# Performance work log

Measured on AMD Instinct MI355X. Metric: run time of the kernel, lower is better.

The kernel has to match this reference:

```python
import jax, jax.numpy as jnp
import numpy as np

N_HEAD = 16
ROPE_BASE = 10000.0


def _rope(x, cos, sin):
    # x: [B,H,T,D]; cos/sin: [T,D/2] broadcast over B,H
    half = x.shape[-1] // 2
    x1, x2 = x[..., :half], x[..., half:]
    return jnp.concatenate([x1 * cos - x2 * sin, x1 * sin + x2 * cos], axis=-1)


def setup_inputs() -> dict:
    key = jax.random.key(0)
    k1, k2, k3 = jax.random.split(key, 3)
    C = 2048
    x = jax.random.normal(k1, (4, 2048, C), dtype=jnp.float32)
    w_qkv = jax.random.normal(k2, (C, 3 * C), dtype=jnp.float32) * 0.02
    w_proj = jax.random.normal(k3, (C, C), dtype=jnp.float32) * 0.02
    return {"x": x, "w_qkv": w_qkv, "w_proj": w_proj}


def reference(x, w_qkv, w_proj):
    B, T, C = x.shape
    H = N_HEAD
    D = C // H
    half = D // 2

    qkv = x @ w_qkv  # [B,T,3C]
    q, k, v = jnp.split(qkv, 3, axis=-1)
    # [B,T,C] -> [B,H,T,D]
    q = q.reshape(B, T, H, D).transpose(0, 2, 1, 3)
    k = k.reshape(B, T, H, D).transpose(0, 2, 1, 3)
    v = v.reshape(B, T, H, D).transpose(0, 2, 1, 3)

    # RoPE cache (start_pos = 0, no kv_cache / prefill path)
    inv_freq = 1.0 / (ROPE_BASE ** (jnp.arange(half, dtype=jnp.float32) / half))
    pos = jnp.arange(T, dtype=jnp.float32)
    freqs = pos[:, None] * inv_freq[None, :]  # [T, half]
    cos, sin = jnp.cos(freqs), jnp.sin(freqs)

    q = _rope(q, cos, sin)
    k = _rope(k, cos, sin)

    # scaled dot-product attention with explicit causal mask
    att = jnp.einsum("bhqd,bhkd->bhqk", q, k) / jnp.sqrt(jnp.asarray(D, x.dtype))
    causal = jnp.arange(T)[:, None] >= jnp.arange(T)[None, :]  # [T,T] bool
    att = jnp.where(causal, att, jnp.asarray(-jnp.inf, att.dtype))
    att = jax.nn.softmax(att, axis=-1)
    # dropout = identity (eval mode)
    out = jnp.einsum("bhqk,bhkd->bhqd", att, v)
    out = out.transpose(0, 2, 1, 3).reshape(B, T, C)
    out = out @ w_proj
    return out, k, v  # (output, new kv-cache)
```

## Files before the change

### kernel.cpp

```cpp
#include <hip/hip_runtime.h>
#include <math.h>

#define CDIM 2048
#define TDIM 2048
#define BDIM 4
#define HDIM 16
#define DDIM 128
#define M1   (BDIM * TDIM)
#define N1   (3 * CDIM)
#define KK   CDIM
#define NT   32

typedef unsigned short u16;
typedef __bf16 bf16x8 __attribute__((ext_vector_type(8)));
typedef float f32x4 __attribute__((ext_vector_type(4)));

__device__ __forceinline__ u16 f2b(float f) {
  union { float f; unsigned u; } x; x.f = f;
  unsigned r = x.u + 0x7fffu + ((x.u >> 16) & 1u);
  return (u16)(r >> 16);
}

__device__ __forceinline__ void gload_lds16(const void* g, void* l) {
  __builtin_amdgcn_global_load_lds(
      (__attribute__((address_space(1))) void*)g,
      (__attribute__((address_space(3))) void*)l, 16, 0, 0);
}

__global__ void convert_x(const float* __restrict__ x, u16* __restrict__ xb, int n4) {
  int i = blockIdx.x * blockDim.x + threadIdx.x;
  if (i < n4) {
    float4 v = ((const float4*)x)[i];
    unsigned long long o = (unsigned long long)f2b(v.x)
                         | ((unsigned long long)f2b(v.y) << 16)
                         | ((unsigned long long)f2b(v.z) << 32)
                         | ((unsigned long long)f2b(v.w) << 48);
    ((unsigned long long*)xb)[i] = o;
  }
}

__global__ void transpose_w(const float* __restrict__ w, u16* __restrict__ wt, int K, int N) {
  __shared__ float tile[32][33];
  const int n0 = blockIdx.x * 32, k0 = blockIdx.y * 32;
  const int tx = threadIdx.x & 31, ty = threadIdx.x >> 5;
  for (int r = ty; r < 32; r += 8)
    tile[r][tx] = w[(k0 + r) * N + n0 + tx];
  __syncthreads();
  for (int r = ty; r < 32; r += 8)
    wt[(n0 + r) * K + k0 + tx] = f2b(tile[tx][r]);
}

__global__ void rope_tab(float* __restrict__ cosT, float* __restrict__ sinT) {
  int i = blockIdx.x * blockDim.x + threadIdx.x;
  int t = i >> 6, d = i & 63;
  double inv = pow(10000.0, -(double)d / 64.0);
  double a = (double)t * inv;
  cosT[i] = (float)cos(a);
  sinT[i] = (float)sin(a);
}

__global__ void transpose_v(const float* __restrict__ v, u16* __restrict__ vt) {
  __shared__ float tile[32][33];
  const int bh = blockIdx.z;
  const int t0 = blockIdx.x * 32, d0 = blockIdx.y * 32;
  const int tx = threadIdx.x & 31, ty = threadIdx.x >> 5;
  const float* src = v + (bh * TDIM + t0) * DDIM + d0;
  for (int r = ty; r < 32; r += 8)
    tile[r][tx] = src[r * DDIM + tx];
  __syncthreads();
  u16* dst = vt + (bh * DDIM + d0) * TDIM + t0;
  for (int r = ty; r < 32; r += 8)
    dst[r * TDIM + tx] = f2b(tile[tx][r]);
}


#define GEMM256_MAINLOOP(APTR, BPTR)                                           \
  const int rA = lane >> 3, cA = lane & 7;                                     \
  const int stgrow = wave * 8 + rA;                                            \
  const int stgoff = stgrow * KK + ((cA ^ rA) * 8);                            \
  const u16* Ag = (APTR) + m0 * KK + stgoff;                                   \
  const u16* Bg = (BPTR) + n0 * KK + stgoff;                                   \
  const int ldsw = wave * 512;                                  \
  f32x4 acc[8][4];                                                             \
  {                                                                            \
    f32x4 z = {0.f, 0.f, 0.f, 0.f};                                            \
    _Pragma("unroll")                                                          \
    for (int i = 0; i < 8; ++i)                                                \
      _Pragma("unroll")                                                        \
      for (int j = 0; j < 4; ++j) acc[i][j] = z;                               \
  }                                                                            \
                                         \
  _Pragma("unroll")                                                            \
  for (int i = 0; i < 4; ++i) {                                                \
    gload_lds16(Ag + i * 64 * KK, &lds[i * 4096 + ldsw]);                      \
    gload_lds16(Bg + i * 64 * KK, &lds[32768 + i * 4096 + ldsw]);              \
  }                                                                            \
  __syncthreads();                                                             \
  const int rsw = c16 & 7;                               \
  for (int kt = 0; kt < NT; ++kt) {                                            \
    const int cur = kt & 1;                                                    \
    const u16* bufA = &lds[cur * 16384];                                       \
    const u16* bufB = &lds[32768 + cur * 16384];                               \
    u16* nA = &lds[(cur ^ 1) * 16384];                                         \
    u16* nB = &lds[32768 + (cur ^ 1) * 16384];                                 \
    const u16* Agn = Ag + (kt + 1) * 64;                                       \
    const u16* Bgn = Bg + (kt + 1) * 64;                                       \
    const bool pre = (kt + 1 < NT);                                            \
    bf16x8 afr[4][2], bfr[2][2], bfr2[2][2];                                   \
                                          \
    _Pragma("unroll")                                                          \
    for (int i = 0; i < 4; ++i)                                                \
      _Pragma("unroll")                                                        \
      for (int kh = 0; kh < 2; ++kh)                                           \
        afr[i][kh] = *(const bf16x8*)&bufA[(wm + i * 16 + c16) * 64 +          \
                                           (((kh * 4 + quad) ^ rsw) * 8)];     \
    _Pragma("unroll")                                                          \
    for (int j = 0; j < 2; ++j)                                                \
      _Pragma("unroll")                                                        \
      for (int kh = 0; kh < 2; ++kh)                                           \
        bfr[j][kh] = *(const bf16x8*)&bufB[(wn + j * 16 + c16) * 64 +          \
                                           (((kh * 4 + quad) ^ rsw) * 8)];     \
    if (pre) {                                                                 \
      _Pragma("unroll")                                                        \
      for (int i = 0; i < 4; ++i)                                              \
        gload_lds16(Agn + i * 64 * KK, &nA[i * 4096 + ldsw]);                  \
    }                                                                          \
    __builtin_amdgcn_s_barrier();                                              \
    asm volatile("s_waitcnt lgkmcnt(0)" ::: "memory");                         \
    __builtin_amdgcn_s_setprio(1);                                             \
    _Pragma("unroll")                                                          \
    for (int i = 0; i < 4; ++i)                                                \
      _Pragma("unroll")                                                        \
      for (int j = 0; j < 2; ++j)                                              \
        _Pragma("unroll")                                                      \
        for (int kh = 0; kh < 2; ++kh)                                         \
          acc[i][j] = __builtin_amdgcn_mfma_f32_16x16x32_bf16(                 \
              afr[i][kh], bfr[j][kh], acc[i][j], 0, 0, 0);                     \
    __builtin_amdgcn_s_setprio(0);                                             \
    __builtin_amdgcn_s_barrier();                                              \
                                          \
    _Pragma("unroll")                                                          \
    for (int j = 0; j < 2; ++j)                                                \
      _Pragma("unroll")                                                        \
      for (int kh = 0; kh < 2; ++kh)                                           \
        bfr2[j][kh] = *(const bf16x8*)&bufB[(wn + (2 + j) * 16 + c16) * 64 +   \
                                            (((kh * 4 + quad) ^ rsw) * 8)];    \
    if (pre) {                                                                 \
      _Pragma("unroll")                                                        \
      for (int i = 0; i < 4; ++i)                                              \
        gload_lds16(Bgn + i * 64 * KK, &nB[i * 4096 + ldsw]);                  \
    }                                                                          \
    __builtin_amdgcn_s_barrier();                                              \
    asm volatile("s_waitcnt lgkmcnt(0)" ::: "memory");                         \
    __builtin_amdgcn_s_setprio(1);                                             \
    _Pragma("unroll")                                                          \
    for (int i = 0; i < 4; ++i)                                                \
      _Pragma("unroll")                                                        \
      for (int j = 0; j < 2; ++j)                                              \
        _Pragma("unroll")                                                      \
        for (int kh = 0; kh < 2; ++kh)                                         \
          acc[i][2 + j] = __builtin_amdgcn_mfma_f32_16x16x32_bf16(             \
              afr[i][kh], bfr2[j][kh], acc[i][2 + j], 0, 0, 0);                \
    __builtin_amdgcn_s_setprio(0);                                             \
    __builtin_amdgcn_s_barrier();                                              \
                                          \
    _Pragma("unroll")                                                          \
    for (int i = 0; i < 4; ++i)                                                \
      _Pragma("unroll")                                                        \
      for (int kh = 0; kh < 2; ++kh)                                           \
        afr[i][kh] = *(const bf16x8*)&bufA[(wm + (4 + i) * 16 + c16) * 64 +    \
                                           (((kh * 4 + quad) ^ rsw) * 8)];     \
    __builtin_amdgcn_s_barrier();                                              \
    asm volatile("s_waitcnt lgkmcnt(0)" ::: "memory");                         \
    __builtin_amdgcn_s_setprio(1);                                             \
    _Pragma("unroll")                                                          \
    for (int i = 0; i < 4; ++i)                                                \
      _Pragma("unroll")                                                        \
      for (int j = 0; j < 2; ++j)                                              \
        _Pragma("unroll")                                                      \
        for (int kh = 0; kh < 2; ++kh)                                         \
          acc[4 + i][2 + j] = __builtin_amdgcn_mfma_f32_16x16x32_bf16(         \
              afr[i][kh], bfr2[j][kh], acc[4 + i][2 + j], 0, 0, 0);            \
    __builtin_amdgcn_s_setprio(0);                                             \
    __builtin_amdgcn_s_barrier();                                              \
                                          \
    _Pragma("unroll")                                                          \
    for (int j = 0; j < 2; ++j)                                                \
      _Pragma("unroll")                                                        \
      for (int kh = 0; kh < 2; ++kh)                                           \
        bfr[j][kh] = *(const bf16x8*)&bufB[(wn + j * 16 + c16) * 64 +          \
                                           (((kh * 4 + quad) ^ rsw) * 8)];     \
    __builtin_amdgcn_s_barrier();                                              \
    asm volatile("s_waitcnt lgkmcnt(0)" ::: "memory");                         \
    __builtin_amdgcn_s_setprio(1);                                             \
    _Pragma("unroll")                                                          \
    for (int i = 0; i < 4; ++i)                                                \
      _Pragma("unroll")                                                        \
      for (int j = 0; j < 2; ++j)                                              \
        _Pragma("unroll")                                                      \
        for (int kh = 0; kh < 2; ++kh)                                         \
          acc[4 + i][j] = __builtin_amdgcn_mfma_f32_16x16x32_bf16(             \
              afr[i][kh], bfr[j][kh], acc[4 + i][j], 0, 0, 0);                 \
    __builtin_amdgcn_s_setprio(0);                                             \
        \
    __syncthreads();                                                           \
  }

__global__ __launch_bounds__(512, 2) void gemm_qkv(
    const u16* __restrict__ A,
    const u16* __restrict__ Bt,
    const float* __restrict__ cosT, const float* __restrict__ sinT,
    u16* __restrict__ qb, u16* __restrict__ kb,
    float* __restrict__ kout, float* __restrict__ vout)
{
  extern __shared__ __align__(16) u16 lds[];
  const int tid = threadIdx.x, wave = tid >> 6, lane = tid & 63;
  const int quad = lane >> 4, c16 = lane & 15;
  const int bid = blockIdx.y * 24 + blockIdx.x;
  const int swz = (bid & 7) * 96 + (bid >> 3);
  const int m0 = (swz / 24) * 256, n0 = (swz % 24) * 256;
  const int wm = (wave >> 2) * 128, wn = (wave & 3) * 64;

  GEMM256_MAINLOOP(A, Bt)

  float* cbuf = (float*)lds;
  const int mat = n0 >> 11;
  const int hbase = (n0 & 2047) >> 7;
  const float qscale = 0.088388347648318447f;
#pragma unroll
  for (int pass = 0; pass < 4; ++pass) {
    __syncthreads();
    if ((wave >> 2) == (pass >> 1)) {
#pragma unroll
      for (int i = 0; i < 4; ++i) {
        const int mf = (pass & 1) * 4 + i;
#pragma unroll
        for (int j = 0; j < 4; ++j)
#pragma unroll
          for (int r = 0; r < 4; ++r)
            cbuf[(i * 16 + quad * 4 + r) * 260 + wn + j * 16 + c16] = acc[mf][j][r];
      }
    }
    __syncthreads();
#pragma unroll
    for (int it = 0; it < 16; ++it) {
      int p = it * 512 + tid;
      int lr = p >> 7;
      int hc = (p >> 6) & 1;
      int d = p & 63;
      float x1 = cbuf[lr * 260 + hc * 128 + d];
      float x2 = cbuf[lr * 260 + hc * 128 + 64 + d];
      int mg = m0 + pass * 64 + lr;
      int b = mg >> 11, t = mg & 2047;
      int h = hbase + hc;
      int idx = ((b * HDIM + h) * TDIM + t) * DDIM + d;
      if (mat == 2) {
        vout[idx] = x1; vout[idx + 64] = x2;
      } else {
        float cs = cosT[t * 64 + d], sn = sinT[t * 64 + d];
        float o1 = x1 * cs - x2 * sn;
        float o2 = x1 * sn + x2 * cs;
        if (mat == 0) {
          qb[idx] = f2b(o1 * qscale); qb[idx + 64] = f2b(o2 * qscale);
        } else {
          kout[idx] = o1; kout[idx + 64] = o2;
          kb[idx] = f2b(o1); kb[idx + 64] = f2b(o2);
        }
      }
    }
  }
}

__global__ __launch_bounds__(512, 2) void gemm_proj(
    const u16* __restrict__ A,
    const u16* __restrict__ Bt,
    float* __restrict__ out)
{
  extern __shared__ __align__(16) u16 lds[];
  const int tid = threadIdx.x, wave = tid >> 6, lane = tid & 63;
  const int quad = lane >> 4, c16 = lane & 15;
  const int bid = blockIdx.y * 8 + blockIdx.x;
  const int swz = (bid & 7) * 32 + (bid >> 3);
  const int m0 = (swz >> 3) * 256, n0 = (swz & 7) * 256;
  const int wm = (wave >> 2) * 128, wn = (wave & 3) * 64;

  GEMM256_MAINLOOP(A, Bt)

#pragma unroll
  for (int mf = 0; mf < 8; ++mf)
#pragma unroll
    for (int nf = 0; nf < 4; ++nf)
#pragma unroll
      for (int r = 0; r < 4; ++r)
        out[(m0 + wm + mf * 16 + quad * 4 + r) * CDIM + n0 + wn + nf * 16 + c16] =
            acc[mf][nf][r];
}

__global__ __launch_bounds__(256, 2) void attn(
    const u16* __restrict__ qb, const u16* __restrict__ kb,
    const u16* __restrict__ vt, u16* __restrict__ att)
{
  __shared__ __attribute__((aligned(16))) u16 sh[24576];
  u16* const ksm = sh;
  u16* const vsm = sh + 8192;
  u16* const psm = sh + 16384;

  const int tid = threadIdx.x, wave = tid >> 6, lane = tid & 63;
  const int quad = lane >> 4, c16 = lane & 15;
  const int bx = blockIdx.x;
  const int bh = blockIdx.y;

  for (int hv = 0; hv < 2; ++hv) {
    const int qt = hv ? (7 - bx) : (bx + 8);
    const int q0 = qt * 128;

    {
      const u16* qg = qb + (bh * TDIM + q0) * DDIM;
      const int rowl = wave * 4 + (lane >> 4);
      const int ch = lane & 15;
#pragma unroll
      for (int r = 0; r < 8; ++r) {
        int row = r * 16 + rowl;
        gload_lds16(qg + row * DDIM + (ch ^ (row & 15)) * 8,
                    &sh[(r * 16 + wave * 4) * 128]);
      }
    }
    __syncthreads();
    bf16x8 qf[2][4];
#pragma unroll
    for (int g = 0; g < 2; ++g)
#pragma unroll
      for (int kp = 0; kp < 4; ++kp)
        qf[g][kp] = *(const bf16x8*)&sh[(g * 64 + wave * 16 + c16) * 128 +
                                        (((kp * 4 + quad) ^ c16) * 8)];
    __syncthreads();

    f32x4 o[2][8];
    f32x4 zero = {0.f, 0.f, 0.f, 0.f};
#pragma unroll
    for (int g = 0; g < 2; ++g)
#pragma unroll
      for (int jd = 0; jd < 8; ++jd) o[g][jd] = zero;
    float mrow[2][4], lrow[2][4];
#pragma unroll
    for (int g = 0; g < 2; ++g)
#pragma unroll
      for (int r = 0; r < 4; ++r) { mrow[g][r] = -INFINITY; lrow[g][r] = 0.f; }

    const int nchunk = 2 * qt + 2;
    for (int kc = 0; kc < nchunk; ++kc) {
      const int kc0 = kc * 64;
      {
        const u16* kg = kb + (bh * TDIM + kc0) * DDIM;
        const int rowl = wave * 4 + (lane >> 4);
        const int ch = lane & 15;
#pragma unroll
        for (int r = 0; r < 4; ++r) {
          int row = r * 16 + rowl;
          gload_lds16(kg + row * DDIM + (ch ^ (row & 15)) * 8,
                      &ksm[(r * 16 + wave * 4) * 128]);
        }
        const u16* vg = vt + bh * (DDIM * TDIM) + kc0;
        const int rowv = wave * 8 + (lane >> 3);
        const int chv = lane & 7;
#pragma unroll
        for (int r = 0; r < 4; ++r) {
          int row = r * 32 + rowv;
          gload_lds16(vg + row * TDIM + (chv ^ (row & 7)) * 8,
                      &vsm[(r * 32 + wave * 8) * 64]);
        }
      }
      __syncthreads();

      f32x4 st[2][4];
#pragma unroll
      for (int g = 0; g < 2; ++g)
#pragma unroll
        for (int j = 0; j < 4; ++j) st[g][j] = zero;
#pragma unroll
      for (int kp = 0; kp < 4; ++kp) {
#pragma unroll
        for (int j = 0; j < 4; ++j) {
          bf16x8 bk = *(const bf16x8*)&ksm[(j * 16 + c16) * 128 +
                                           (((kp * 4 + quad) ^ c16) * 8)];
          st[0][j] = __builtin_amdgcn_mfma_f32_16x16x32_bf16(qf[0][kp], bk, st[0][j], 0, 0, 0);
          st[1][j] = __builtin_amdgcn_mfma_f32_16x16x32_bf16(qf[1][kp], bk, st[1][j], 0, 0, 0);
        }
      }

      u16* const pw = psm + wave * 2048;
      float al2[2][4];
#pragma unroll
      for (int g = 0; g < 2; ++g) {
        const bool dg = (kc >= 2 * qt + g);
        const int qrow_base = q0 + g * 64 + wave * 16 + quad * 4;
#pragma unroll
        for (int r = 0; r < 4; ++r) {
          float mx = -INFINITY;
#pragma unroll
          for (int j = 0; j < 4; ++j) {
            float sv = st[g][j][r];
            if (dg && (kc0 + j * 16 + c16 > qrow_base + r)) sv = -INFINITY;
            st[g][j][r] = sv;
            mx = fmaxf(mx, sv);
          }
          mx = fmaxf(mx, __shfl_xor(mx, 1, 64));
          mx = fmaxf(mx, __shfl_xor(mx, 2, 64));
          mx = fmaxf(mx, __shfl_xor(mx, 4, 64));
          mx = fmaxf(mx, __shfl_xor(mx, 8, 64));
          float mnew = fmaxf(mrow[g][r], mx);
          float al = __expf(mrow[g][r] - mnew);
          mrow[g][r] = mnew;
          al2[g][r] = al;
          float sum = 0.f;
          const int row16 = quad * 4 + r;
#pragma unroll
          for (int j = 0; j < 4; ++j) {
            float p = __expf(st[g][j][r] - mnew);
            sum += p;
            int chunk = (j * 2 + (c16 >> 3)) ^ (row16 & 7);
            pw[g * 1024 + row16 * 64 + chunk * 8 + (c16 & 7)] = f2b(p);
          }
          sum += __shfl_xor(sum, 1, 64);
          sum += __shfl_xor(sum, 2, 64);
          sum += __shfl_xor(sum, 4, 64);
          sum += __shfl_xor(sum, 8, 64);
          lrow[g][r] = lrow[g][r] * al + sum;
        }
#pragma unroll
        for (int jd = 0; jd < 8; ++jd)
#pragma unroll
          for (int r = 0; r < 4; ++r)
            o[g][jd][r] *= al2[g][r];
      }

      asm volatile("s_waitcnt lgkmcnt(0)" ::: "memory");

#pragma unroll
      for (int s = 0; s < 2; ++s) {
        const int chp = ((s * 4 + quad) ^ (c16 & 7)) * 8;
        bf16x8 ap0 = *(const bf16x8*)&pw[c16 * 64 + chp];
        bf16x8 ap1 = *(const bf16x8*)&pw[1024 + c16 * 64 + chp];
#pragma unroll
        for (int jd = 0; jd < 8; ++jd) {
          bf16x8 bv = *(const bf16x8*)&vsm[(jd * 16 + c16) * 64 + chp];
          o[0][jd] = __builtin_amdgcn_mfma_f32_16x16x32_bf16(ap0, bv, o[0][jd], 0, 0, 0);
          o[1][jd] = __builtin_amdgcn_mfma_f32_16x16x32_bf16(ap1, bv, o[1][jd], 0, 0, 0);
        }
      }
      __syncthreads();
    }

    const int b = bh >> 4, h = bh & 15;
#pragma unroll
    for (int g = 0; g < 2; ++g) {
      float ri[4];
#pragma unroll
      for (int r = 0; r < 4; ++r) ri[r] = 1.f / lrow[g][r];
#pragma unroll
      for (int jd = 0; jd < 8; ++jd)
#pragma unroll
        for (int r = 0; r < 4; ++r) {
          int t = q0 + g * 64 + wave * 16 + quad * 4 + r;
          att[(b * TDIM + t) * CDIM + h * DDIM + jd * 16 + c16] = f2b(o[g][jd][r] * ri[r]);
        }
    }
  }
}

extern "C" void kernel_launch(void* const* d_in, const int* in_sizes, int n_in,
                              void* d_out, int out_size, void* d_ws, size_t ws_size,
                              hipStream_t stream) {
  (void)in_sizes; (void)n_in; (void)out_size; (void)ws_size;
  const float* x      = (const float*)d_in[0];
  const float* w_qkv  = (const float*)d_in[1];
  const float* w_proj = (const float*)d_in[2];
  float* out  = (float*)d_out;
  float* kout = out + 16777216;
  float* vout = out + 2 * 16777216;

  char* ws = (char*)d_ws;
  u16*   xb     = (u16*)(ws);
  u16*   wqkvT  = (u16*)(ws + 33554432);
  u16*   wprojT = (u16*)(ws + 58720256);
  float* cosT   = (float*)(ws + 67108864);
  float* sinT   = (float*)(ws + 67633152);
  u16*   qb     = (u16*)(ws + 68157440);
  u16*   kb     = (u16*)(ws + 101711872);
  u16*   vt     = (u16*)(ws + 135266304);
  u16*   att    = xb;

  static int attr_set = 0;
  if (!attr_set) {
    hipFuncSetAttribute((const void*)gemm_qkv,
                        hipFuncAttributeMaxDynamicSharedMemorySize, 131072);
    hipFuncSetAttribute((const void*)gemm_proj,
                        hipFuncAttributeMaxDynamicSharedMemorySize, 131072);
    attr_set = 1;
  }

  convert_x<<<16384, 256, 0, stream>>>(x, xb, 4194304);
  transpose_w<<<dim3(192, 64), 256, 0, stream>>>(w_qkv, wqkvT, KK, N1);
  transpose_w<<<dim3(64, 64), 256, 0, stream>>>(w_proj, wprojT, KK, CDIM);
  rope_tab<<<512, 256, 0, stream>>>(cosT, sinT);
  gemm_qkv<<<dim3(24, 32), 512, 131072, stream>>>(xb, wqkvT, cosT, sinT, qb, kb, kout, vout);
  transpose_v<<<dim3(64, 4, 64), 256, 0, stream>>>(vout, vt);
  attn<<<dim3(8, 64), 256, 0, stream>>>(qb, kb, vt, att);
  gemm_proj<<<dim3(8, 32), 512, 131072, stream>>>(att, wprojT, out);
}
```

Baseline: 784.6 us.

## Stage GEMM tile loads per quarter with fine-grained vmcnt waits instead of full syncs

Restructures the 256x256 GEMM main loop so the next K-tile's global-to-LDS loads are issued in quarter-sized chunks, each interleaved with one MFMA phase. The LDS layout is permuted so each chunk maps to the rows consumed in a specific phase. Per-phase s_waitcnt vmcnt waits plus s_barrier replace the end-of-iteration __syncthreads, and the last iteration is peeled to drain the pipeline. The goal is finer overlap of memory traffic with MFMA work and less barrier stall, at the cost of fragile hand-counted wait counts and row remapping that must match the epilogue.

After: 767.2 us. -2.2%, faster.

```diff
diff --git a/kernel.cpp b/kernel.cpp
--- a/kernel.cpp
+++ b/kernel.cpp
@@ -74,56 +74,32 @@
 }
 
 
-#define GEMM256_MAINLOOP(APTR, BPTR)                                           \
-  const int rA = lane >> 3, cA = lane & 7;                                     \
-  const int stgrow = wave * 8 + rA;                                            \
-  const int stgoff = stgrow * KK + ((cA ^ rA) * 8);                            \
-  const u16* Ag = (APTR) + m0 * KK + stgoff;                                   \
-  const u16* Bg = (BPTR) + n0 * KK + stgoff;                                   \
-  const int ldsw = wave * 512;                                  \
-  f32x4 acc[8][4];                                                             \
+#define VMW4 asm volatile("s_waitcnt vmcnt(4)" ::: "memory");
+#define VMW2 asm volatile("s_waitcnt vmcnt(2)" ::: "memory");
+#define VMW0 asm volatile("s_waitcnt vmcnt(0)" ::: "memory");
+#define NOWAIT
+
+#define GEMM256_ITER(bufA_, bufB_, nA_, nB_, kno_, STG, W0, W1, W3)            \
   {                                                                            \
-    f32x4 z = {0.f, 0.f, 0.f, 0.f};                                            \
-    _Pragma("unroll")                                                          \
-    for (int i = 0; i < 8; ++i)                                                \
-      _Pragma("unroll")                                                        \
-      for (int j = 0; j < 4; ++j) acc[i][j] = z;                               \
-  }                                                                            \
-                                         \
-  _Pragma("unroll")                                                            \
-  for (int i = 0; i < 4; ++i) {                                                \
-    gload_lds16(Ag + i * 64 * KK, &lds[i * 4096 + ldsw]);                      \
-    gload_lds16(Bg + i * 64 * KK, &lds[32768 + i * 4096 + ldsw]);              \
-  }                                                                            \
-  __syncthreads();                                                             \
-  const int rsw = c16 & 7;                               \
-  for (int kt = 0; kt < NT; ++kt) {                                            \
-    const int cur = kt & 1;                                                    \
-    const u16* bufA = &lds[cur * 16384];                                       \
-    const u16* bufB = &lds[32768 + cur * 16384];                               \
-    u16* nA = &lds[(cur ^ 1) * 16384];                                         \
-    u16* nB = &lds[32768 + (cur ^ 1) * 16384];                                 \
-    const u16* Agn = Ag + (kt + 1) * 64;                                       \
-    const u16* Bgn = Bg + (kt + 1) * 64;                                       \
-    const bool pre = (kt + 1 < NT);                                            \
     bf16x8 afr[4][2], bfr[2][2], bfr2[2][2];                                   \
-                                          \
+      \
     _Pragma("unroll")                                                          \
     for (int i = 0; i < 4; ++i)                                                \
       _Pragma("unroll")                                                        \
       for (int kh = 0; kh < 2; ++kh)                                           \
-        afr[i][kh] = *(const bf16x8*)&bufA[(wm + i * 16 + c16) * 64 +          \
-                                           (((kh * 4 + quad) ^ rsw) * 8)];     \
+        afr[i][kh] = *(const bf16x8*)&(bufA_)[aoff + i * 1024 +                \
+                                              (((kh * 4 + quad) ^ rsw) * 8)];  \
     _Pragma("unroll")                                                          \
     for (int j = 0; j < 2; ++j)                                                \
       _Pragma("unroll")                                                        \
       for (int kh = 0; kh < 2; ++kh)                                           \
-        bfr[j][kh] = *(const bf16x8*)&bufB[(wn + j * 16 + c16) * 64 +          \
-                                           (((kh * 4 + quad) ^ rsw) * 8)];     \
-    if (pre) {                                                                 \
-      _Pragma("unroll")                                                        \
-      for (int i = 0; i < 4; ++i)                                              \
-        gload_lds16(Agn + i * 64 * KK, &nA[i * 4096 + ldsw]);                  \
+        bfr[j][kh] = *(const bf16x8*)&(bufB_)[boff + j * 1024 +                \
+                                              (((kh * 4 + quad) ^ rsw) * 8)];  \
+    if (STG) {                                                                 \
+      _Pragma("unroll")                                                        \
+      for (int q = 0; q < 2; ++q)                                              \
+        gload_lds16(AgBase + (q * 128) * KK + (kno_),                          \
+                    &(nA_)[q * 4096 + ldsw]);                                  \
     }                                                                          \
     __builtin_amdgcn_s_barrier();                                              \
     asm volatile("s_waitcnt lgkmcnt(0)" ::: "memory");                         \
@@ -137,18 +113,20 @@
           acc[i][j] = __builtin_amdgcn_mfma_f32_16x16x32_bf16(                 \
               afr[i][kh], bfr[j][kh], acc[i][j], 0, 0, 0);                     \
     __builtin_amdgcn_s_setprio(0);                                             \
-    __builtin_amdgcn_s_barrier();                                              \
-                                          \
+    W0                                                                         \
+    __builtin_amdgcn_s_barrier();                                              \
+      \
     _Pragma("unroll")                                                          \
     for (int j = 0; j < 2; ++j)                                                \
       _Pragma("unroll")                                                        \
       for (int kh = 0; kh < 2; ++kh)                                           \
-        bfr2[j][kh] = *(const bf16x8*)&bufB[(wn + (2 + j) * 16 + c16) * 64 +   \
-                                            (((kh * 4 + quad) ^ rsw) * 8)];    \
-    if (pre) {                                                                 \
-      _Pragma("unroll")                                                        \
-      for (int i = 0; i < 4; ++i)                                              \
-        gload_lds16(Bgn + i * 64 * KK, &nB[i * 4096 + ldsw]);                  \
+        bfr2[j][kh] = *(const bf16x8*)&(bufB_)[8192 + boff + j * 1024 +        \
+                                               (((kh * 4 + quad) ^ rsw) * 8)]; \
+    if (STG) {                                                                 \
+      _Pragma("unroll")                                                        \
+      for (int q = 0; q < 2; ++q)                                              \
+        gload_lds16(BgBase + (q * 128) * KK + (kno_),                          \
+                    &(nB_)[q * 4096 + ldsw]);                                  \
     }                                                                          \
     __builtin_amdgcn_s_barrier();                                              \
     asm volatile("s_waitcnt lgkmcnt(0)" ::: "memory");                         \
@@ -162,14 +140,21 @@
           acc[i][2 + j] = __builtin_amdgcn_mfma_f32_16x16x32_bf16(             \
               afr[i][kh], bfr2[j][kh], acc[i][2 + j], 0, 0, 0);                \
     __builtin_amdgcn_s_setprio(0);                                             \
-    __builtin_amdgcn_s_barrier();                                              \
-                                          \
+    W1                                                                         \
+    __builtin_amdgcn_s_barrier();                                              \
+      \
     _Pragma("unroll")                                                          \
     for (int i = 0; i < 4; ++i)                                                \
       _Pragma("unroll")                                                        \
       for (int kh = 0; kh < 2; ++kh)                                           \
-        afr[i][kh] = *(const bf16x8*)&bufA[(wm + (4 + i) * 16 + c16) * 64 +    \
-                                           (((kh * 4 + quad) ^ rsw) * 8)];     \
+        afr[i][kh] = *(const bf16x8*)&(bufA_)[8192 + aoff + i * 1024 +         \
+                                              (((kh * 4 + quad) ^ rsw) * 8)];  \
+    if (STG) {                                                                 \
+      _Pragma("unroll")                                                        \
+      for (int q = 0; q < 2; ++q)                                              \
+        gload_lds16(BgBase + (q * 128 + 32) * KK + (kno_),                     \
+                    &(nB_)[8192 + q * 4096 + ldsw]);                           \
+    }                                                                          \
     __builtin_amdgcn_s_barrier();                                              \
     asm volatile("s_waitcnt lgkmcnt(0)" ::: "memory");                         \
     __builtin_amdgcn_s_setprio(1);                                             \
@@ -183,13 +168,19 @@
               afr[i][kh], bfr2[j][kh], acc[4 + i][2 + j], 0, 0, 0);            \
     __builtin_amdgcn_s_setprio(0);                                             \
     __builtin_amdgcn_s_barrier();                                              \
-                                          \
+      \
     _Pragma("unroll")                                                          \
     for (int j = 0; j < 2; ++j)                                                \
       _Pragma("unroll")                                                        \
       for (int kh = 0; kh < 2; ++kh)                                           \
-        bfr[j][kh] = *(const bf16x8*)&bufB[(wn + j * 16 + c16) * 64 +          \
-                                           (((kh * 4 + quad) ^ rsw) * 8)];     \
+        bfr[j][kh] = *(const bf16x8*)&(bufB_)[boff + j * 1024 +                \
+                                              (((kh * 4 + quad) ^ rsw) * 8)];  \
+    if (STG) {                                                                 \
+      _Pragma("unroll")                                                        \
+      for (int q = 0; q < 2; ++q)                                              \
+        gload_lds16(AgBase + (q * 128 + 64) * KK + (kno_),                     \
+                    &(nA_)[8192 + q * 4096 + ldsw]);                           \
+    }                                                                          \
     __builtin_amdgcn_s_barrier();                                              \
     asm volatile("s_waitcnt lgkmcnt(0)" ::: "memory");                         \
     __builtin_amdgcn_s_setprio(1);                                             \
@@ -202,9 +193,57 @@
           acc[4 + i][j] = __builtin_amdgcn_mfma_f32_16x16x32_bf16(             \
               afr[i][kh], bfr[j][kh], acc[4 + i][j], 0, 0, 0);                 \
     __builtin_amdgcn_s_setprio(0);                                             \
-        \
-    __syncthreads();                                                           \
+    W3                                                                         \
+    __builtin_amdgcn_s_barrier();                                              \
   }
+
+#define GEMM256_MAINLOOP(APTR, BPTR)                                           \
+  const int rA = lane >> 3, cA = lane & 7;                                     \
+  const int w8r = wave * 8 + rA;                                               \
+  const int swz8 = (cA ^ rA) * 8;                                              \
+  const u16* AgBase = (APTR) + (m0 + w8r) * KK + swz8;                         \
+  const int nb = ((w8r >> 5) * 64) + (w8r & 31);                               \
+  const u16* BgBase = (BPTR) + (n0 + nb) * KK + swz8;                          \
+  const int ldsw = wave * 512;                                                 \
+  const int rsw = c16 & 7;                                                     \
+  const int aoff = (((wave >> 2) * 64) + c16) * 64;                            \
+  const int boff = (((wave & 3) * 32) + c16) * 64;                             \
+  f32x4 acc[8][4];                                                             \
+  {                                                                            \
+    f32x4 z = {0.f, 0.f, 0.f, 0.f};                                            \
+    _Pragma("unroll")                                                          \
+    for (int i = 0; i < 8; ++i)                                                \
+      _Pragma("unroll")                                                        \
+      for (int j = 0; j < 4; ++j) acc[i][j] = z;                               \
+  }                                                                            \
+                  \
+  _Pragma("unroll")                                                            \
+  for (int q = 0; q < 2; ++q)                                                  \
+    gload_lds16(AgBase + (q * 128) * KK, &lds[q * 4096 + ldsw]);               \
+  _Pragma("unroll")                                                            \
+  for (int q = 0; q < 2; ++q)                                                  \
+    gload_lds16(BgBase + (q * 128) * KK, &lds[32768 + q * 4096 + ldsw]);       \
+  _Pragma("unroll")                                                            \
+  for (int q = 0; q < 2; ++q)                                                  \
+    gload_lds16(BgBase + (q * 128 + 32) * KK,                                  \
+                &lds[32768 + 8192 + q * 4096 + ldsw]);                         \
+  _Pragma("unroll")                                                            \
+  for (int q = 0; q < 2; ++q)                                                  \
+    gload_lds16(AgBase + (q * 128 + 64) * KK, &lds[8192 + q * 4096 + ldsw]);   \
+  VMW4                                                                         \
+  __builtin_amdgcn_s_barrier();                                                \
+  for (int kt = 0; kt < NT - 1; ++kt) {                                        \
+    const int cur = kt & 1;                                                    \
+    const u16* bA = &lds[cur * 16384];                                         \
+    const u16* bB = &lds[32768 + cur * 16384];                                 \
+    u16* nA = &lds[(cur ^ 1) * 16384];                                         \
+    u16* nB = &lds[32768 + (cur ^ 1) * 16384];                                 \
+    const int kno = (kt + 1) * 64;                                             \
+    GEMM256_ITER(bA, bB, nA, nB, kno, 1, VMW4, VMW4, VMW4)                     \
+  }                                                                            \
+                    \
+  GEMM256_ITER((&lds[16384]), (&lds[32768 + 16384]), (&lds[0]),                \
+               (&lds[32768]), 0, 0, VMW2, VMW0, NOWAIT)
 
 __global__ __launch_bounds__(512, 2) void gemm_qkv(
     const u16* __restrict__ A,
@@ -220,6 +259,7 @@
   const int swz = (bid & 7) * 96 + (bid >> 3);
   const int m0 = (swz / 24) * 256, n0 = (swz % 24) * 256;
   const int wm = (wave >> 2) * 128, wn = (wave & 3) * 64;
+  (void)wm; (void)wn;
 
   GEMM256_MAINLOOP(A, Bt)
 
@@ -238,7 +278,7 @@
         for (int j = 0; j < 4; ++j)
 #pragma unroll
           for (int r = 0; r < 4; ++r)
-            cbuf[(i * 16 + quad * 4 + r) * 260 + wn + j * 16 + c16] = acc[mf][j][r];
+            cbuf[(i * 16 + quad * 4 + r) * 260 + (wave & 3) * 64 + j * 16 + c16] = acc[mf][j][r];
       }
     }
     __syncthreads();
```
